# Optimization experiments

Measured on AMD Instinct MI355X. Metric: run time of the kernel, lower is better.

## Reference

```python
import jax, jax.numpy as jnp
import numpy as np
import math

HIDDEN = 1024
HEADS = 16
HEAD_DIM = HIDDEN // HEADS


def setup_inputs() -> dict:
    key = jax.random.key(0)
    ks = jax.random.split(key, 9)
    s = 1.0 / math.sqrt(HIDDEN)
    x = jax.random.normal(ks[0], (4, 2048, HIDDEN), dtype=jnp.float32)
    Wq = jax.random.uniform(ks[1], (HIDDEN, HIDDEN), jnp.float32, -s, s)
    bq = jax.random.uniform(ks[2], (HIDDEN,), jnp.float32, -s, s)
    Wk = jax.random.uniform(ks[3], (HIDDEN, HIDDEN), jnp.float32, -s, s)
    bk = jax.random.uniform(ks[4], (HIDDEN,), jnp.float32, -s, s)
    Wv = jax.random.uniform(ks[5], (HIDDEN, HIDDEN), jnp.float32, -s, s)
    bv = jax.random.uniform(ks[6], (HIDDEN,), jnp.float32, -s, s)
    Wo = jax.random.uniform(ks[7], (HIDDEN, HIDDEN), jnp.float32, -s, s)
    bo = jax.random.uniform(ks[8], (HIDDEN,), jnp.float32, -s, s)
    return {"x": x, "Wq": Wq, "bq": bq, "Wk": Wk, "bk": bk,
            "Wv": Wv, "bv": bv, "Wo": Wo, "bo": bo}


def reference(x, Wq, bq, Wk, bk, Wv, bv, Wo, bo):
    B, T, D = x.shape
    H, Hd = HEADS, HEAD_DIM
    scale = 1.0 / math.sqrt(Hd)
    # projections (torch Linear: y = x @ W.T + b)
    q = (x @ Wq.T + bq).reshape(B, T, H, Hd).transpose(0, 2, 1, 3)  # [B,H,T,Hd]
    k = (x @ Wk.T + bk).reshape(B, T, H, Hd).transpose(0, 2, 1, 3)
    v = (x @ Wv.T + bv).reshape(B, T, H, Hd).transpose(0, 2, 1, 3)
    scores = jnp.einsum("bhqd,bhkd->bhqk", q, k) * scale  # [B,H,T,T]
    attn = jax.nn.softmax(scores, axis=-1)
    out = jnp.einsum("bhqk,bhkd->bhqd", attn, v)  # [B,H,T,Hd]
    out = out.transpose(0, 2, 1, 3).reshape(B, T, D)
    out = out @ Wo.T + bo
    return out.mean(axis=1)  # [B, D]
```

## Files before the change

kernel.cpp:

```cpp
#include <hip/hip_runtime.h>
#include <stdint.h>

#define HIDDEN 1024
#define HEADS 16
#define HEAD_DIM 64
#define BATCH 4
#define SEQ 2048
#define NTOK (BATCH * SEQ)

typedef __attribute__((ext_vector_type(8))) short bf16x8;
typedef __attribute__((ext_vector_type(4))) float floatx4;
typedef __attribute__((ext_vector_type(16))) float floatx16;

#define SCALE_Q 0.18033688011112042f

__device__ __forceinline__ unsigned short f2bf(float f) {
    union { float f; unsigned u; } x; x.f = f;
    unsigned r = x.u + 0x7fffu + ((x.u >> 16) & 1u);
    return (unsigned short)(r >> 16);
}

__device__ __forceinline__ float fast_exp2(float x) {
#if __has_builtin(__builtin_amdgcn_exp2f)
    return __builtin_amdgcn_exp2f(x);
#else
    return exp2f(x);
#endif
}

typedef __attribute__((address_space(3))) unsigned int lds_u32;
typedef const __attribute__((address_space(1))) unsigned int gl_u32;

__device__ __forceinline__ void async_cp16(const void* g, void* l) {
#if __has_builtin(__builtin_amdgcn_global_load_lds)
    __builtin_amdgcn_global_load_lds((gl_u32*)g, (lds_u32*)l, 16, 0, 0);
#else
    *(uint4*)((char*)l + (threadIdx.x & 63) * 16) = *(const uint4*)g;
#endif
}

__global__ __launch_bounds__(256) void conv_all(
    const float* __restrict__ x, const float* __restrict__ Wq,
    const float* __restrict__ Wk, const float* __restrict__ Wv,
    unsigned short* __restrict__ x_bf, unsigned short* __restrict__ wq_bf,
    unsigned short* __restrict__ wk_bf, unsigned short* __restrict__ wv_bf,
    float* __restrict__ accp) {
    const int blk = blockIdx.x, tid = threadIdx.x;
    const float* src;
    unsigned short* dst;
    size_t i;
    if (blk < 8192) {
        src = x; dst = x_bf; i = (size_t)blk * 256 + tid;
        if (blk < 16) accp[blk * 256 + tid] = 0.0f;
    } else {
        int r = blk - 8192;
        int s = r >> 10;
        src = (s == 0) ? Wq : (s == 1) ? Wk : Wv;
        dst = (s == 0) ? wq_bf : (s == 1) ? wk_bf : wv_bf;
        i = (size_t)(r & 1023) * 256 + tid;
    }
    float4 v = *(const float4*)(src + 4 * i);
    unsigned short o[4];
    o[0] = f2bf(v.x); o[1] = f2bf(v.y); o[2] = f2bf(v.z); o[3] = f2bf(v.w);
    *(ushort4*)(dst + 4 * i) = *(ushort4*)o;
}

__global__ __launch_bounds__(256, 3) void qkv_gemm(
    const unsigned short* __restrict__ X,
    const unsigned short* __restrict__ W0, const unsigned short* __restrict__ W1,
    const unsigned short* __restrict__ W2,
    const float* __restrict__ b0, const float* __restrict__ b1,
    const float* __restrict__ b2,
    unsigned short* __restrict__ O0, unsigned short* __restrict__ O1,
    unsigned short* __restrict__ O2) {
    __shared__ unsigned short Alds[2][4096];
    __shared__ unsigned short Blds[2][4096];

    const int id = blockIdx.x;
    const int y = id >> 6;
    const int z = y >> 3;
    const int n0 = (y & 7) * 128;
    const int m0 = (id & 63) * 128;
    const unsigned short* W = (z == 0) ? W0 : (z == 1) ? W1 : W2;
    const float* bias       = (z == 0) ? b0 : (z == 1) ? b1 : b2;
    unsigned short* O       = (z == 0) ? O0 : (z == 1) ? O1 : O2;

    const int tid = threadIdx.x, lane = tid & 63, wave = tid >> 6;
    const int mw = (wave >> 1) * 64, nw = (wave & 1) * 64;

    const int sr = lane >> 2;
    const int scb = (lane & 3) * 8;
    const unsigned short* ga[2];
    const unsigned short* gb[2];
#pragma unroll
    for (int j = 0; j < 2; ++j) {
        ga[j] = X + (size_t)(m0 + wave * 32 + j * 16 + sr) * HIDDEN + scb;
        gb[j] = W + (size_t)(n0 + wave * 32 + j * 16 + sr) * HIDDEN + scb;
    }

    floatx4 acc[4][4];
#pragma unroll
    for (int tm = 0; tm < 4; ++tm)
#pragma unroll
        for (int tn = 0; tn < 4; ++tn)
#pragma unroll
            for (int r = 0; r < 4; ++r) acc[tm][tn][r] = 0.f;

#pragma unroll
    for (int j = 0; j < 2; ++j) {
        async_cp16(ga[j], (char*)Alds[0] + wave * 2048 + j * 1024);
        async_cp16(gb[j], (char*)Blds[0] + wave * 2048 + j * 1024);
        ga[j] += 32; gb[j] += 32;
    }
    __syncthreads();

    const int frag_off = (lane & 15) * 64 + (lane >> 4) * 16;
    for (int kt = 0; kt < 32; ++kt) {
        const int cur = kt & 1;
        if (kt < 31) {
#pragma unroll
            for (int j = 0; j < 2; ++j) {
                async_cp16(ga[j], (char*)Alds[cur ^ 1] + wave * 2048 + j * 1024);
                async_cp16(gb[j], (char*)Blds[cur ^ 1] + wave * 2048 + j * 1024);
                ga[j] += 32; gb[j] += 32;
            }
        }
        bf16x8 af[4], bfr[4];
#pragma unroll
        for (int t = 0; t < 4; ++t) {
            af[t]  = *(bf16x8*)((char*)Alds[cur] + (mw + t * 16) * 64 + frag_off);
            bfr[t] = *(bf16x8*)((char*)Blds[cur] + (nw + t * 16) * 64 + frag_off);
        }
#pragma unroll
        for (int tm = 0; tm < 4; ++tm)
#pragma unroll
            for (int tn = 0; tn < 4; ++tn)
                acc[tm][tn] = __builtin_amdgcn_mfma_f32_16x16x32_bf16(af[tm], bfr[tn], acc[tm][tn], 0, 0, 0);
        if (kt < 31) __syncthreads();
    }

    const int col = lane & 15, rbase = (lane >> 4) * 4;
#pragma unroll
    for (int tm = 0; tm < 4; ++tm) {
#pragma unroll
        for (int tn = 0; tn < 4; ++tn) {
            const int n = n0 + nw + tn * 16 + col;
            const float bs = bias[n];
            const int m_base = m0 + mw + tm * 16 + rbase;
            if (z == 2) {
                const int hh = n >> 6, dd = n & 63;
                const int bb = m_base >> 11, tt = m_base & (SEQ - 1);
                unsigned short vals[4];
#pragma unroll
                for (int r = 0; r < 4; ++r) vals[r] = f2bf(acc[tm][tn][r] + bs);
                *(ushort4*)&O[(((size_t)bb * HEADS + hh) * HEAD_DIM + dd) * SEQ + tt] = *(ushort4*)vals;
            } else {
                const float sc = (z == 0) ? SCALE_Q : 1.0f;
#pragma unroll
                for (int r = 0; r < 4; ++r)
                    O[(size_t)(m_base + r) * HIDDEN + n] = f2bf((acc[tm][tn][r] + bs) * sc);
            }
        }
    }
}

__global__ __launch_bounds__(256, 2) void attn_mfma(
    const unsigned short* __restrict__ Q, const unsigned short* __restrict__ K,
    const unsigned short* __restrict__ Vt, float* __restrict__ accp) {
    __shared__ unsigned short Klds[2][8192];
    __shared__ unsigned short Vlds[2][8192];

    const int tid = threadIdx.x, lane = tid & 63, wave = tid >> 6;
    const int lq = lane & 31, g2 = lane >> 5;

    const int f = blockIdx.x;
    const int bh = (f & 7) * 8 + ((f >> 3) & 7);
    const int qc = f >> 6;
    const int b = bh >> 4, h = bh & 15;

    bf16x8 qfrag[2][4];
#pragma unroll
    for (int g = 0; g < 2; ++g) {
        const size_t qb = ((size_t)(b * SEQ + qc * 256 + wave * 64 + g * 32 + lq)) * HIDDEN
                          + h * HEAD_DIM + g2 * 8;
#pragma unroll
        for (int ds = 0; ds < 4; ++ds) qfrag[g][ds] = *(const bf16x8*)&Q[qb + ds * 16];
    }

    const unsigned short* kg[4];
    const unsigned short* vg[4];
    {
        const int kr = lane >> 3;
        const int kc = ((lane & 7) ^ kr) * 8;
#pragma unroll
        for (int j = 0; j < 4; ++j)
            kg[j] = K + ((size_t)(b * SEQ + wave * 32 + j * 8 + kr)) * HIDDEN + h * HEAD_DIM + kc;
#pragma unroll
        for (int j = 0; j < 4; ++j) {
            const int dl = wave * 16 + j * 4 + (lane >> 4);
            const int cc = ((lane & 15) ^ (dl & 15)) * 8;
            vg[j] = Vt + ((size_t)bh * HEAD_DIM + dl) * SEQ + cc;
        }
    }

    floatx16 oacc[2][2], lacc[2];
#pragma unroll
    for (int g = 0; g < 2; ++g)
#pragma unroll
        for (int r = 0; r < 16; ++r) { oacc[g][0][r] = 0.f; oacc[g][1][r] = 0.f; lacc[g][r] = 0.f; }

    bf16x8 ones;
    {
        union { bf16x8 v; unsigned u[4]; } o;
        o.u[0] = o.u[1] = o.u[2] = o.u[3] = 0x3F803F80u;
        ones = o.v;
    }

#pragma unroll
    for (int j = 0; j < 4; ++j) {
        async_cp16(kg[j], (char*)Klds[0] + (wave * 32 + j * 8) * 128);
        async_cp16(vg[j], (char*)Vlds[0] + (wave * 16 + j * 4) * 256);
        kg[j] += 128 * HIDDEN; vg[j] += 128;
    }
    __syncthreads();

    for (int it = 0; it < 16; ++it) {
        const int cur = it & 1;
        if (it < 15) {
#pragma unroll
            for (int j = 0; j < 4; ++j) {
                async_cp16(kg[j], (char*)Klds[cur ^ 1] + (wave * 32 + j * 8) * 128);
                async_cp16(vg[j], (char*)Vlds[cur ^ 1] + (wave * 16 + j * 4) * 256);
                kg[j] += 128 * HIDDEN; vg[j] += 128;
            }
        }
#pragma unroll
        for (int ks4 = 0; ks4 < 4; ++ks4) {
            const int kk = ks4 * 32;
            const int rr = kk + lq;
            bf16x8 kf[4];
#pragma unroll
            for (int ds = 0; ds < 4; ++ds)
                kf[ds] = *(bf16x8*)((char*)Klds[cur] + rr * 128 + (((g2 + 2 * ds) ^ (lq & 7)) * 16));

            unsigned pk[2][8];
#pragma unroll
            for (int g = 0; g < 2; ++g) {
                floatx16 sacc;
#pragma unroll
                for (int r = 0; r < 16; ++r) sacc[r] = 0.f;
#pragma unroll
                for (int ds = 0; ds < 4; ++ds)
                    sacc = __builtin_amdgcn_mfma_f32_32x32x16_bf16(kf[ds], qfrag[g][ds], sacc, 0, 0, 0);
#pragma unroll
                for (int j = 0; j < 8; ++j) {
                    union { float f; unsigned u; } plo, phi;
                    plo.f = fast_exp2(sacc[2 * j]);
                    phi.f = fast_exp2(sacc[2 * j + 1]);
                    pk[g][j] = __builtin_amdgcn_perm(phi.u, plo.u, 0x07060302u);
                }
            }
#pragma unroll
            for (int ks2 = 0; ks2 < 2; ++ks2) {
                bf16x8 vf[2];
#pragma unroll
                for (int nf = 0; nf < 2; ++nf) {
                    const int d = nf * 32 + lq;
                    const int c0 = (4 * ks4 + 2 * ks2) ^ (d & 15);
                    const int c1 = (4 * ks4 + 2 * ks2 + 1) ^ (d & 15);
                    union { uint2 h[2]; bf16x8 v; } u;
                    u.h[0] = *(uint2*)((char*)Vlds[cur] + d * 256 + c0 * 16 + g2 * 8);
                    u.h[1] = *(uint2*)((char*)Vlds[cur] + d * 256 + c1 * 16 + g2 * 8);
                    vf[nf] = u.v;
                }
#pragma unroll
                for (int g = 0; g < 2; ++g) {
                    union { uint4 u; bf16x8 v; } af;
                    af.u.x = pk[g][4 * ks2];
                    af.u.y = pk[g][4 * ks2 + 1];
                    af.u.z = pk[g][4 * ks2 + 2];
                    af.u.w = pk[g][4 * ks2 + 3];
#pragma unroll
                    for (int nf = 0; nf < 2; ++nf)
                        oacc[g][nf] = __builtin_amdgcn_mfma_f32_32x32x16_bf16(af.v, vf[nf], oacc[g][nf], 0, 0, 0);
                    lacc[g] = __builtin_amdgcn_mfma_f32_32x32x16_bf16(af.v, ones, lacc[g], 0, 0, 0);
                }
            }
        }
        if (it < 15) __syncthreads();
    }

#pragma unroll
    for (int g = 0; g < 2; ++g)
#pragma unroll
        for (int nf = 0; nf < 2; ++nf) {
            float v = 0.f;
#pragma unroll
            for (int r = 0; r < 16; ++r) v += oacc[g][nf][r] / lacc[g][r];
            v += __shfl_xor(v, 32, 64);
            if (lane < 32)
                atomicAdd(&accp[b * HIDDEN + h * HEAD_DIM + nf * 32 + lq], v);
        }
}

__global__ __launch_bounds__(256) void out_proj(const float* __restrict__ acc,
                                                const float* __restrict__ Wo,
                                                const float* __restrict__ bo,
                                                float* __restrict__ out) {
    const int n = blockIdx.x * 256 + threadIdx.x;
    const int b = blockIdx.y;
    const float invT = 1.0f / (float)SEQ;
    float s = 0.f;
    for (int k = 0; k < HIDDEN; k += 4) {
        float4 w = *(const float4*)&Wo[(size_t)n * HIDDEN + k];
        float4 a = *(const float4*)&acc[b * HIDDEN + k];
        s += w.x * a.x + w.y * a.y + w.z * a.z + w.w * a.w;
    }
    out[b * HIDDEN + n] = s * invT + bo[n];
}

extern "C" void kernel_launch(void* const* d_in, const int* in_sizes, int n_in,
                              void* d_out, int out_size, void* d_ws, size_t ws_size,
                              hipStream_t stream) {
    const float* x  = (const float*)d_in[0];
    const float* Wq = (const float*)d_in[1];
    const float* bq = (const float*)d_in[2];
    const float* Wk = (const float*)d_in[3];
    const float* bk = (const float*)d_in[4];
    const float* Wv = (const float*)d_in[5];
    const float* bv = (const float*)d_in[6];
    const float* Wo = (const float*)d_in[7];
    const float* bo = (const float*)d_in[8];
    float* out = (float*)d_out;

    char* ws = (char*)d_ws;
    unsigned short* x_bf  = (unsigned short*)(ws);
    unsigned short* wq_bf = (unsigned short*)(ws + 16777216);
    unsigned short* wk_bf = (unsigned short*)(ws + 18874368);
    unsigned short* wv_bf = (unsigned short*)(ws + 20971520);
    unsigned short* q_bf  = (unsigned short*)(ws + 23068672);
    unsigned short* k_bf  = (unsigned short*)(ws + 39845888);
    unsigned short* vt_bf = (unsigned short*)(ws + 56623104);
    float*          accp  = (float*)(ws + 73400320);

    conv_all<<<dim3(8192 + 3072), dim3(256), 0, stream>>>(
        x, Wq, Wk, Wv, x_bf, wq_bf, wk_bf, wv_bf, accp);

    qkv_gemm<<<dim3(64 * 24), dim3(256), 0, stream>>>(
        x_bf, wq_bf, wk_bf, wv_bf, bq, bk, bv, q_bf, k_bf, vt_bf);

    attn_mfma<<<dim3(512), dim3(256), 0, stream>>>(q_bf, k_bf, vt_bf, accp);

    out_proj<<<dim3(HIDDEN / 256, BATCH), dim3(256), 0, stream>>>(accp, Wo, bo, out);
}
```

Measured before the change: 266.2 us.

## Fuse Q/K/V projections per block sharing X tile and re-swizzle V layout

After: 269.3 us. Within noise of the previous version (+1.2%).

```diff
diff --git a/kernel.cpp b/kernel.cpp
--- a/kernel.cpp
+++ b/kernel.cpp
@@ -65,7 +65,7 @@
     *(ushort4*)(dst + 4 * i) = *(ushort4*)o;
 }
 
-__global__ __launch_bounds__(256, 3) void qkv_gemm(
+__global__ __launch_bounds__(256, 2) void qkv_gemm(
     const unsigned short* __restrict__ X,
     const unsigned short* __restrict__ W0, const unsigned short* __restrict__ W1,
     const unsigned short* __restrict__ W2,
@@ -74,43 +74,53 @@
     unsigned short* __restrict__ O0, unsigned short* __restrict__ O1,
     unsigned short* __restrict__ O2) {
     __shared__ unsigned short Alds[2][4096];
-    __shared__ unsigned short Blds[2][4096];
+    __shared__ unsigned short Blds[2][6144];
 
     const int id = blockIdx.x;
-    const int y = id >> 6;
-    const int z = y >> 3;
-    const int n0 = (y & 7) * 128;
-    const int m0 = (id & 63) * 128;
-    const unsigned short* W = (z == 0) ? W0 : (z == 1) ? W1 : W2;
-    const float* bias       = (z == 0) ? b0 : (z == 1) ? b1 : b2;
-    unsigned short* O       = (z == 0) ? O0 : (z == 1) ? O1 : O2;
+    const int mb = id & 63, nb = id >> 6;
+    const int m0 = mb * 128, n0 = nb * 64;
 
     const int tid = threadIdx.x, lane = tid & 63, wave = tid >> 6;
-    const int mw = (wave >> 1) * 64, nw = (wave & 1) * 64;
-
-    const int sr = lane >> 2;
-    const int scb = (lane & 3) * 8;
+
+    const unsigned short* WZ0 = W0;
+    const unsigned short* WZ1 = W1;
+    const unsigned short* WZ2 = W2;
+
     const unsigned short* ga[2];
-    const unsigned short* gb[2];
-#pragma unroll
-    for (int j = 0; j < 2; ++j) {
-        ga[j] = X + (size_t)(m0 + wave * 32 + j * 16 + sr) * HIDDEN + scb;
-        gb[j] = W + (size_t)(n0 + wave * 32 + j * 16 + sr) * HIDDEN + scb;
-    }
-
-    floatx4 acc[4][4];
-#pragma unroll
-    for (int tm = 0; tm < 4; ++tm)
-#pragma unroll
-        for (int tn = 0; tn < 4; ++tn)
-#pragma unroll
-            for (int r = 0; r < 4; ++r) acc[tm][tn][r] = 0.f;
+#pragma unroll
+    for (int j = 0; j < 2; ++j)
+        ga[j] = X + (size_t)(m0 + wave * 32 + j * 16 + (lane >> 2)) * HIDDEN + (lane & 3) * 8;
+
+    const unsigned short* gb[3];
+    int bdst[3];
+#pragma unroll
+    for (int jj = 0; jj < 3; ++jj) {
+        const int i = wave * 3 + jj;
+        const int z = i >> 2, seg = i & 3;
+        const unsigned short* Wz = (z == 0) ? WZ0 : (z == 1) ? WZ1 : WZ2;
+        gb[jj] = Wz + (size_t)(n0 + seg * 16 + (lane >> 2)) * HIDDEN + (lane & 3) * 8;
+        bdst[jj] = z * 4096 + seg * 1024;
+    }
+
+    floatx4 acc[3][2][4];
+#pragma unroll
+    for (int z = 0; z < 3; ++z)
+#pragma unroll
+        for (int tm = 0; tm < 2; ++tm)
+#pragma unroll
+            for (int tn = 0; tn < 4; ++tn)
+#pragma unroll
+                for (int r = 0; r < 4; ++r) acc[z][tm][tn][r] = 0.f;
 
 #pragma unroll
     for (int j = 0; j < 2; ++j) {
         async_cp16(ga[j], (char*)Alds[0] + wave * 2048 + j * 1024);
-        async_cp16(gb[j], (char*)Blds[0] + wave * 2048 + j * 1024);
-        ga[j] += 32; gb[j] += 32;
+        ga[j] += 32;
+    }
+#pragma unroll
+    for (int jj = 0; jj < 3; ++jj) {
+        async_cp16(gb[jj], (char*)Blds[0] + bdst[jj]);
+        gb[jj] += 32;
     }
     __syncthreads();
 
@@ -121,44 +131,61 @@
 #pragma unroll
             for (int j = 0; j < 2; ++j) {
                 async_cp16(ga[j], (char*)Alds[cur ^ 1] + wave * 2048 + j * 1024);
-                async_cp16(gb[j], (char*)Blds[cur ^ 1] + wave * 2048 + j * 1024);
-                ga[j] += 32; gb[j] += 32;
-            }
-        }
-        bf16x8 af[4], bfr[4];
-#pragma unroll
-        for (int t = 0; t < 4; ++t) {
-            af[t]  = *(bf16x8*)((char*)Alds[cur] + (mw + t * 16) * 64 + frag_off);
-            bfr[t] = *(bf16x8*)((char*)Blds[cur] + (nw + t * 16) * 64 + frag_off);
-        }
-#pragma unroll
-        for (int tm = 0; tm < 4; ++tm)
+                ga[j] += 32;
+            }
+#pragma unroll
+            for (int jj = 0; jj < 3; ++jj) {
+                async_cp16(gb[jj], (char*)Blds[cur ^ 1] + bdst[jj]);
+                gb[jj] += 32;
+            }
+        }
+        bf16x8 af[2];
+#pragma unroll
+        for (int tm = 0; tm < 2; ++tm)
+            af[tm] = *(bf16x8*)((char*)Alds[cur] + (wave * 32 + tm * 16) * 64 + frag_off);
+#pragma unroll
+        for (int z = 0; z < 3; ++z) {
+            bf16x8 bfr[4];
 #pragma unroll
             for (int tn = 0; tn < 4; ++tn)
-                acc[tm][tn] = __builtin_amdgcn_mfma_f32_16x16x32_bf16(af[tm], bfr[tn], acc[tm][tn], 0, 0, 0);
+                bfr[tn] = *(bf16x8*)((char*)Blds[cur] + z * 4096 + tn * 1024 + frag_off);
+#pragma unroll
+            for (int tm = 0; tm < 2; ++tm)
+#pragma unroll
+                for (int tn = 0; tn < 4; ++tn)
+                    acc[z][tm][tn] = __builtin_amdgcn_mfma_f32_16x16x32_bf16(af[tm], bfr[tn], acc[z][tm][tn], 0, 0, 0);
+        }
         if (kt < 31) __syncthreads();
     }
 
     const int col = lane & 15, rbase = (lane >> 4) * 4;
 #pragma unroll
-    for (int tm = 0; tm < 4; ++tm) {
-#pragma unroll
-        for (int tn = 0; tn < 4; ++tn) {
-            const int n = n0 + nw + tn * 16 + col;
-            const float bs = bias[n];
-            const int m_base = m0 + mw + tm * 16 + rbase;
-            if (z == 2) {
-                const int hh = n >> 6, dd = n & 63;
-                const int bb = m_base >> 11, tt = m_base & (SEQ - 1);
-                unsigned short vals[4];
-#pragma unroll
-                for (int r = 0; r < 4; ++r) vals[r] = f2bf(acc[tm][tn][r] + bs);
-                *(ushort4*)&O[(((size_t)bb * HEADS + hh) * HEAD_DIM + dd) * SEQ + tt] = *(ushort4*)vals;
-            } else {
-                const float sc = (z == 0) ? SCALE_Q : 1.0f;
-#pragma unroll
-                for (int r = 0; r < 4; ++r)
-                    O[(size_t)(m_base + r) * HIDDEN + n] = f2bf((acc[tm][tn][r] + bs) * sc);
+    for (int z = 0; z < 3; ++z) {
+        const float* bias = (z == 0) ? b0 : (z == 1) ? b1 : b2;
+        unsigned short* O = (z == 0) ? O0 : (z == 1) ? O1 : O2;
+        const float sc = (z == 0) ? SCALE_Q : 1.0f;
+#pragma unroll
+        for (int tm = 0; tm < 2; ++tm) {
+#pragma unroll
+            for (int tn = 0; tn < 4; ++tn) {
+                const int n = n0 + tn * 16 + col;
+                const float bs = bias[n];
+                const int m_base = m0 + wave * 32 + tm * 16 + rbase;
+                if (z == 2) {
+                    const int hh = n >> 6, dd = n & 63;
+                    const int bb = m_base >> 11, tt = m_base & (SEQ - 1);
+                    const int tb = tt >> 7, gg = (tt & 127) >> 2;
+                    const int gr = (gg + dd) & 31;
+                    unsigned short vals[4];
+#pragma unroll
+                    for (int r = 0; r < 4; ++r) vals[r] = f2bf(acc[z][tm][tn][r] + bs);
+                    *(ushort4*)&O[(((size_t)bb * HEADS + hh) * HEAD_DIM + dd) * SEQ + tb * 128 + gr * 4] =
+                        *(ushort4*)vals;
+                } else {
+#pragma unroll
+                    for (int r = 0; r < 4; ++r)
+                        O[(size_t)(m_base + r) * HIDDEN + n] = f2bf((acc[z][tm][tn][r] + bs) * sc);
+                }
             }
         }
     }
@@ -198,8 +225,7 @@
 #pragma unroll
         for (int j = 0; j < 4; ++j) {
             const int dl = wave * 16 + j * 4 + (lane >> 4);
-            const int cc = ((lane & 15) ^ (dl & 15)) * 8;
-            vg[j] = Vt + ((size_t)bh * HEAD_DIM + dl) * SEQ + cc;
+            vg[j] = Vt + ((size_t)bh * HEAD_DIM + dl) * SEQ + (lane & 15) * 8;
         }
     }
 
@@ -262,15 +288,16 @@
             }
 #pragma unroll
             for (int ks2 = 0; ks2 < 2; ++ks2) {
+                const int gran0 = 8 * ks4 + 4 * ks2 + g2;
                 bf16x8 vf[2];
 #pragma unroll
                 for (int nf = 0; nf < 2; ++nf) {
                     const int d = nf * 32 + lq;
-                    const int c0 = (4 * ks4 + 2 * ks2) ^ (d & 15);
-                    const int c1 = (4 * ks4 + 2 * ks2 + 1) ^ (d & 15);
+                    const int p0 = (gran0 + d) & 31;
+                    const int p1 = (gran0 + 2 + d) & 31;
                     union { uint2 h[2]; bf16x8 v; } u;
-                    u.h[0] = *(uint2*)((char*)Vlds[cur] + d * 256 + c0 * 16 + g2 * 8);
-                    u.h[1] = *(uint2*)((char*)Vlds[cur] + d * 256 + c1 * 16 + g2 * 8);
+                    u.h[0] = *(uint2*)((char*)Vlds[cur] + d * 256 + p0 * 8);
+                    u.h[1] = *(uint2*)((char*)Vlds[cur] + d * 256 + p1 * 8);
                     vf[nf] = u.v;
                 }
 #pragma unroll
@@ -346,7 +373,7 @@
     conv_all<<<dim3(8192 + 3072), dim3(256), 0, stream>>>(
         x, Wq, Wk, Wv, x_bf, wq_bf, wk_bf, wv_bf, accp);
 
-    qkv_gemm<<<dim3(64 * 24), dim3(256), 0, stream>>>(
+    qkv_gemm<<<dim3(1024), dim3(256), 0, stream>>>(
         x_bf, wq_bf, wk_bf, wv_bf, bq, bk, bv, q_bf, k_bf, vt_bf);
 
     attn_mfma<<<dim3(512), dim3(256), 0, stream>>>(q_bf, k_bf, vt_bf, accp);
```
